# Kernel optimization log

Hardware: AMD Instinct MI355X
Metric: run time of the kernel (lower is better)

Reference implementation:

```python
import jax, jax.numpy as jnp
import numpy as np

NUM_GENES = 5000
EMBED = 64
HID = 64
FEATS = 64
SLOPE = 0.01  # nn.LeakyReLU default
BN_EPS = 1e-5


def setup_inputs() -> dict:
    key = jax.random.key(0)
    ks = jax.random.split(key, 20)
    N, E = 40000, 1280000
    def w(k, shape):
        return jax.random.normal(k, shape, dtype=jnp.float32) * 0.05
    inp = {
        "x": jax.random.normal(ks[0], (N, FEATS), dtype=jnp.float32),
        "edge_index": jax.random.randint(ks[1], (2, E), 0, N, dtype=jnp.int64),
        # pre_mp Linear(num_feats, hidden)
        "W_pre": w(ks[2], (FEATS, HID)), "b_pre": w(ks[3], (HID,)),
        # conv 0 MLP: Linear->LeakyReLU->Linear
        "c0_W1": w(ks[4], (HID, HID)), "c0_b1": w(ks[5], (HID,)),
        "c0_W2": w(ks[6], (HID, HID)), "c0_b2": w(ks[7], (HID,)),
        # bn 0 (only bns[0] is used since last conv has no bn)
        "bn0_g": jnp.ones((HID,), jnp.float32), "bn0_b": jnp.zeros((HID,), jnp.float32),
        # conv 1 MLP
        "c1_W1": w(ks[8], (HID, HID)), "c1_b1": w(ks[9], (HID,)),
        "c1_W2": w(ks[10], (HID, HID)), "c1_b2": w(ks[11], (HID,)),
        # post_mp: Linear(hid,hid)->LeakyReLU->Linear(hid,embed)
        "Wp1": w(ks[12], (HID, HID)), "bp1": w(ks[13], (HID,)),
        "Wp2": w(ks[14], (HID, EMBED)), "bp2": w(ks[15], (EMBED,)),
    }
    return inp


def _gin_conv(x, src, dst, W1, b1, W2, b2):
    # GINConv, eps=0: MLP(x + sum_{j in N(i)} x_j)
    agg = jax.ops.segment_sum(x[src], dst, num_segments=x.shape[0])
    h = x + agg
    h = jax.nn.leaky_relu(h @ W1 + b1, SLOPE) @ W2 + b2
    return h


def _batchnorm(h, g, b):
    mu = h.mean(axis=0)
    var = ((h - mu) ** 2).mean(axis=0)  # biased, training-mode BN
    return (h - mu) * jax.lax.rsqrt(var + BN_EPS) * g + b


def reference(x, edge_index, W_pre, b_pre, c0_W1, c0_b1, c0_W2, c0_b2,
              bn0_g, bn0_b, c1_W1, c1_b1, c1_W2, c1_b2, Wp1, bp1, Wp2, bp2):
    src, dst = edge_index[0], edge_index[1]
    h = x @ W_pre + b_pre                                  # [N, HID]
    h = _gin_conv(h, src, dst, c0_W1, c0_b1, c0_W2, c0_b2)
    h = _batchnorm(h, bn0_g, bn0_b)
    h = _gin_conv(h, src, dst, c1_W1, c1_b1, c1_W2, c1_b2)  # last conv, no bn
    h = jax.nn.leaky_relu(h @ Wp1 + bp1, SLOPE) @ Wp2 + bp2  # [N, EMBED]
    # flatten + split into per-graph chunks of num_genes*embed, then stack
    return h.reshape(-1, NUM_GENES * EMBED)                 # [B, 5000*64]
```

## Files before the change

kernel.cpp:

```cpp
#include <hip/hip_runtime.h>
#include <hip/hip_fp16.h>

constexpr float SLOPE  = 0.01f;
constexpr float BN_EPS = 1e-5f;
constexpr int   CAP    = 96;
constexpr int   CLAMP  = 80;
constexpr int   NXCD   = 8;
constexpr int   EPB    = 2048;

__device__ inline void acc8(const uint4& v, float* a) {
    float2 f;
    f = __half22float2(*(const __half2*)&v.x); a[0] += f.x; a[1] += f.y;
    f = __half22float2(*(const __half2*)&v.y); a[2] += f.x; a[3] += f.y;
    f = __half22float2(*(const __half2*)&v.z); a[4] += f.x; a[5] += f.y;
    f = __half22float2(*(const __half2*)&v.w); a[6] += f.x; a[7] += f.y;
}

__global__ void k_fill_linear(const int* __restrict__ src, const int* __restrict__ dst,
                              int* __restrict__ cnt, unsigned short* __restrict__ ssrc, int E,
                              const float* __restrict__ x, const float* __restrict__ W,
                              const float* __restrict__ bias, __half* __restrict__ H0,
                              int total, int fillBlocks, int N, int Npart) {
    int bid = blockIdx.x;
    if (bid < fillBlocks) {
        int p     = bid & (NXCD - 1);
        int chunk = bid >> 3;
        int lo = p * Npart;
        int hi = min(N, lo + Npart);
        int base = chunk * EPB;
#pragma unroll
        for (int i = 0; i < EPB / 256; ++i) {
            int e = base + i * 256 + (int)threadIdx.x;
            if (e < E) {
                int d = dst[e];
                if (d >= lo && d < hi) {
                    int pos = atomicAdd(&cnt[d], 1);
                    if (pos < CAP) ssrc[(size_t)d * CAP + pos] = (unsigned short)src[e];
                }
            }
        }
    } else {
        int gid = (bid - fillBlocks) * 256 + threadIdx.x;
        if (gid < total) {
            int n = gid >> 6, f = gid & 63;
            const float* row = x + (size_t)n * 64;
            float acc = bias[f];
#pragma unroll
            for (int k = 0; k < 64; ++k) acc = fmaf(row[k], W[k * 64 + f], acc);
            H0[gid] = __float2half(acc);
        }
    }
}

#define GLD(j) \
    uint4 vA##j, vB##j; \
    { int jA = sidx[g][((j) << 4) + sub]; \
      int jB = sidx[g][((j) << 4) + 8 + sub]; \
      vA##j = in16[(size_t)jA * 8 + q]; \
      vB##j = in16[(size_t)jB * 8 + q]; }
#define GACC(j) do { acc8(vA##j, a); acc8(vB##j, a); } while (0)

template <bool BN_IN, bool DO_POST, typename TO>
__global__ void k_conv8(const __half* __restrict__ in, const int* __restrict__ cnt,
                        const unsigned short* __restrict__ ssrc,
                        const float* __restrict__ stats, const float* __restrict__ gm,
                        const float* __restrict__ bt, float invN,
                        const float* __restrict__ W1, const float* __restrict__ b1,
                        const float* __restrict__ W2, const float* __restrict__ b2,
                        const float* __restrict__ Wp1, const float* __restrict__ bp1,
                        const float* __restrict__ Wp2, const float* __restrict__ bp2,
                        TO* __restrict__ out, int N, int nblk) {
    __shared__ unsigned short sidx[4][CAP];
    __shared__ float row[4][64];
    __shared__ float t[4][64];
    __shared__ float csc[64], csh[64];

    int bid = blockIdx.x;
    int q8 = nblk / NXCD, r8 = nblk % NXCD;
    int xcd = bid % NXCD, sl = bid / NXCD;
    int wg = (xcd < r8 ? xcd * (q8 + 1) : r8 * (q8 + 1) + (xcd - r8) * q8) + sl;
    int n0 = wg * 4;

    int tid = threadIdx.x;
    int lane = tid & 63, g = tid >> 6;
    int n = n0 + g;
    bool act = n < N;
    int sub = lane >> 3;
    int q   = lane & 7;

    if constexpr (BN_IN) {
        if (tid < 64) {
            float mu  = stats[tid] * invN;
            float var = stats[64 + tid] * invN - mu * mu;
            float sc  = rsqrtf(var + BN_EPS) * gm[tid];
            csc[tid] = sc;
            csh[tid] = bt[tid] - mu * sc;
        }
        __syncthreads();
    }

    if (act) {
        const uint4* in16 = (const uint4*)in;
        int c  = min(cnt[n], CLAMP);
        c = __builtin_amdgcn_readfirstlane(c);
        int cp = (c + 15) & ~15;
        int iters = cp >> 4;

        const unsigned short* bkt = ssrc + (size_t)n * CAP;
        unsigned short self = (unsigned short)n;
        if (lane < cp) sidx[g][lane] = (lane < c) ? bkt[lane] : self;
        int p2 = lane + 64;
        if (p2 < cp) sidx[g][p2] = (p2 < c) ? bkt[p2] : self;

        uint4 vs = make_uint4(0, 0, 0, 0);
        if (sub == 0) vs = in16[(size_t)n * 8 + q];

        float a[8] = {0.f, 0.f, 0.f, 0.f, 0.f, 0.f, 0.f, 0.f};
        switch (iters) {
        case 1: { GLD(0) GACC(0); } break;
        case 2: { GLD(0) GLD(1) GACC(0); GACC(1); } break;
        case 3: { GLD(0) GLD(1) GLD(2) GACC(0); GACC(1); GACC(2); } break;
        case 4: { GLD(0) GLD(1) GLD(2) GACC(0); GLD(3) GACC(1); GACC(2); GACC(3); } break;
        case 5: { GLD(0) GLD(1) GLD(2) GACC(0); GLD(3) GACC(1); GLD(4) GACC(2);
                  GACC(3); GACC(4); } break;
        default: break;
        }
#pragma unroll
        for (int k = 0; k < 8; ++k) {
            a[k] += __shfl_xor(a[k], 8);
            a[k] += __shfl_xor(a[k], 16);
            a[k] += __shfl_xor(a[k], 32);
        }
        if (sub == 0) {
            float ws = 1.0f - (float)(cp - c);
            float2 f;
            f = __half22float2(*(const __half2*)&vs.x); a[0] = fmaf(ws, f.x, a[0]); a[1] = fmaf(ws, f.y, a[1]);
            f = __half22float2(*(const __half2*)&vs.y); a[2] = fmaf(ws, f.x, a[2]); a[3] = fmaf(ws, f.y, a[3]);
            f = __half22float2(*(const __half2*)&vs.z); a[4] = fmaf(ws, f.x, a[4]); a[5] = fmaf(ws, f.y, a[5]);
            f = __half22float2(*(const __half2*)&vs.w); a[6] = fmaf(ws, f.x, a[6]); a[7] = fmaf(ws, f.y, a[7]);
            int f0 = q * 8;
            if constexpr (BN_IN) {
                float dp1 = (float)(c + 1);
#pragma unroll
                for (int k = 0; k < 8; ++k) a[k] = fmaf(csc[f0 + k], a[k], dp1 * csh[f0 + k]);
            }
            *(float4*)&row[g][f0]     = make_float4(a[0], a[1], a[2], a[3]);
            *(float4*)&row[g][f0 + 4] = make_float4(a[4], a[5], a[6], a[7]);
        }

        float a1 = b1[lane];
#pragma unroll
        for (int k0 = 0; k0 < 16; ++k0) {
            float4 r = *(const float4*)&row[g][k0 * 4];
            a1 = fmaf(r.x, W1[(k0 * 4 + 0) * 64 + lane], a1);
            a1 = fmaf(r.y, W1[(k0 * 4 + 1) * 64 + lane], a1);
            a1 = fmaf(r.z, W1[(k0 * 4 + 2) * 64 + lane], a1);
            a1 = fmaf(r.w, W1[(k0 * 4 + 3) * 64 + lane], a1);
        }
        t[g][lane] = a1 > 0.f ? a1 : SLOPE * a1;

        float a2 = b2[lane];
#pragma unroll
        for (int k0 = 0; k0 < 16; ++k0) {
            float4 r = *(const float4*)&t[g][k0 * 4];
            a2 = fmaf(r.x, W2[(k0 * 4 + 0) * 64 + lane], a2);
            a2 = fmaf(r.y, W2[(k0 * 4 + 1) * 64 + lane], a2);
            a2 = fmaf(r.z, W2[(k0 * 4 + 2) * 64 + lane], a2);
            a2 = fmaf(r.w, W2[(k0 * 4 + 3) * 64 + lane], a2);
        }
        if constexpr (!DO_POST) {
            out[(size_t)n * 64 + lane] = (TO)a2;
        } else {
            row[g][lane] = a2;
            float a3 = bp1[lane];
#pragma unroll
            for (int k0 = 0; k0 < 16; ++k0) {
                float4 r = *(const float4*)&row[g][k0 * 4];
                a3 = fmaf(r.x, Wp1[(k0 * 4 + 0) * 64 + lane], a3);
                a3 = fmaf(r.y, Wp1[(k0 * 4 + 1) * 64 + lane], a3);
                a3 = fmaf(r.z, Wp1[(k0 * 4 + 2) * 64 + lane], a3);
                a3 = fmaf(r.w, Wp1[(k0 * 4 + 3) * 64 + lane], a3);
            }
            t[g][lane] = a3 > 0.f ? a3 : SLOPE * a3;

            float a4 = bp2[lane];
#pragma unroll
            for (int k0 = 0; k0 < 16; ++k0) {
                float4 r = *(const float4*)&t[g][k0 * 4];
                a4 = fmaf(r.x, Wp2[(k0 * 4 + 0) * 64 + lane], a4);
                a4 = fmaf(r.y, Wp2[(k0 * 4 + 1) * 64 + lane], a4);
                a4 = fmaf(r.z, Wp2[(k0 * 4 + 2) * 64 + lane], a4);
                a4 = fmaf(r.w, Wp2[(k0 * 4 + 3) * 64 + lane], a4);
            }
            out[(size_t)n * 64 + lane] = (TO)a4;
        }
    }
}

__global__ void k_bn_stats_h(const __half* __restrict__ h, float* __restrict__ stats, int N) {
    int f = threadIdx.x & 63, g = threadIdx.x >> 6;
    float s = 0.f, ss = 0.f;
    for (int r = blockIdx.x * 4 + g; r < N; r += gridDim.x * 4) {
        float v = __half2float(h[(size_t)r * 64 + f]);
        s += v;
        ss += v * v;
    }
    __shared__ float sh[2][256];
    sh[0][threadIdx.x] = s;
    sh[1][threadIdx.x] = ss;
    __syncthreads();
    if (g == 0) {
        s  = sh[0][f] + sh[0][f + 64] + sh[0][f + 128] + sh[0][f + 192];
        ss = sh[1][f] + sh[1][f + 64] + sh[1][f + 128] + sh[1][f + 192];
        atomicAdd(&stats[f], s);
        atomicAdd(&stats[64 + f], ss);
    }
}

__global__ void k_linear_f(const float* __restrict__ in, const float* __restrict__ W,
                           const float* __restrict__ bias, float* __restrict__ out, int total) {
    int gid = blockIdx.x * blockDim.x + threadIdx.x;
    if (gid >= total) return;
    int n = gid >> 6, f = gid & 63;
    const float* row = in + (size_t)n * 64;
    float acc = bias[f];
#pragma unroll
    for (int k = 0; k < 64; ++k) acc = fmaf(row[k], W[k * 64 + f], acc);
    out[gid] = acc;
}

__global__ void k_scatter(const float* __restrict__ h, const int* __restrict__ src,
                          const int* __restrict__ dst, float* __restrict__ agg, int E) {
    long long gid = (long long)blockIdx.x * blockDim.x + threadIdx.x;
    if (gid >= (long long)E * 64) return;
    int e = (int)(gid >> 6);
    int f = (int)(gid & 63);
    atomicAdd(&agg[(size_t)dst[e] * 64 + f], h[(size_t)src[e] * 64 + f]);
}

__global__ void k_mlp2(const float* __restrict__ in, const float* __restrict__ agg,
                       const float* __restrict__ W1, const float* __restrict__ b1,
                       const float* __restrict__ W2, const float* __restrict__ b2,
                       float* __restrict__ out, int N) {
    __shared__ float row[4][64];
    __shared__ float t[4][64];
    int f = threadIdx.x & 63, g = threadIdx.x >> 6;
    int n = blockIdx.x * 4 + g;
    bool act = n < N;
    if (act) {
        float v = in[(size_t)n * 64 + f];
        if (agg) v += agg[(size_t)n * 64 + f];
        row[g][f] = v;
    }
    __syncthreads();
    if (act) {
        float acc = b1[f];
#pragma unroll
        for (int k = 0; k < 64; ++k) acc = fmaf(row[g][k], W1[k * 64 + f], acc);
        t[g][f] = acc > 0.f ? acc : SLOPE * acc;
    }
    __syncthreads();
    if (act) {
        float acc = b2[f];
#pragma unroll
        for (int k = 0; k < 64; ++k) acc = fmaf(t[g][k], W2[k * 64 + f], acc);
        out[(size_t)n * 64 + f] = acc;
    }
}

__global__ void k_bn_stats_f(const float* __restrict__ h, float* __restrict__ stats, int N) {
    int f = threadIdx.x & 63, g = threadIdx.x >> 6;
    float s = 0.f, ss = 0.f;
    for (int r = blockIdx.x * 4 + g; r < N; r += gridDim.x * 4) {
        float v = h[(size_t)r * 64 + f];
        s += v;
        ss += v * v;
    }
    __shared__ float sh[2][256];
    sh[0][threadIdx.x] = s;
    sh[1][threadIdx.x] = ss;
    __syncthreads();
    if (g == 0) {
        s  = sh[0][f] + sh[0][f + 64] + sh[0][f + 128] + sh[0][f + 192];
        ss = sh[1][f] + sh[1][f + 64] + sh[1][f + 128] + sh[1][f + 192];
        atomicAdd(&stats[f], s);
        atomicAdd(&stats[64 + f], ss);
    }
}

__global__ void k_bn_apply(float* __restrict__ h, const float* __restrict__ stats,
                           const float* __restrict__ gm, const float* __restrict__ bt,
                           int total, float invN) {
    int gid = blockIdx.x * blockDim.x + threadIdx.x;
    if (gid >= total) return;
    int f = gid & 63;
    float mu  = stats[f] * invN;
    float var = stats[64 + f] * invN - mu * mu;
    float sc  = rsqrtf(var + BN_EPS) * gm[f];
    h[gid] = (h[gid] - mu) * sc + bt[f];
}

extern "C" void kernel_launch(void* const* d_in, const int* in_sizes, int n_in,
                              void* d_out, int out_size, void* d_ws, size_t ws_size,
                              hipStream_t stream) {
    const float* x      = (const float*)d_in[0];
    const int*   ei     = (const int*)d_in[1];
    const float* W_pre  = (const float*)d_in[2];
    const float* b_pre  = (const float*)d_in[3];
    const float* c0_W1  = (const float*)d_in[4];
    const float* c0_b1  = (const float*)d_in[5];
    const float* c0_W2  = (const float*)d_in[6];
    const float* c0_b2  = (const float*)d_in[7];
    const float* bn0_g  = (const float*)d_in[8];
    const float* bn0_b  = (const float*)d_in[9];
    const float* c1_W1  = (const float*)d_in[10];
    const float* c1_b1  = (const float*)d_in[11];
    const float* c1_W2  = (const float*)d_in[12];
    const float* c1_b2  = (const float*)d_in[13];
    const float* Wp1    = (const float*)d_in[14];
    const float* bp1    = (const float*)d_in[15];
    const float* Wp2    = (const float*)d_in[16];
    const float* bp2    = (const float*)d_in[17];

    const int N = in_sizes[0] / 64;
    const int E = in_sizes[1] / 2;
    const int total = N * 64;
    const float invN = 1.0f / (float)N;

    const int* src = ei;
    const int* dst = ei + E;

    dim3 blk(256);
    dim3 grid_n((N + 3) / 4);
    int nblk = (N + 3) / 4;
    int Npart = (N + NXCD - 1) / NXCD;
    int fillBlocks = ((E + EPB - 1) / EPB) * NXCD;
    int linBlocks  = (total + 255) / 256;

    char* w = (char*)d_ws;
    __half* H1 = (__half*)w;                     w += (size_t)total * 2;
    w = (char*)(((size_t)w + 255) & ~(size_t)255);
    unsigned short* ssrc = (unsigned short*)w;   w += (size_t)N * CAP * 2 + 128;
    w = (char*)(((size_t)w + 255) & ~(size_t)255);
    int* cnt = (int*)w;                          w += (size_t)N * 4;
    float* stats = (float*)w;                    w += 128 * 4;
    size_t needed = (size_t)(w - (char*)d_ws);

    if (ws_size >= needed) {
        __half* H0 = (__half*)d_out;
        hipMemsetAsync(cnt, 0, (size_t)N * 4, stream);
        k_fill_linear<<<dim3(fillBlocks + linBlocks), blk, 0, stream>>>(
            src, dst, cnt, ssrc, E, x, W_pre, b_pre, H0, total, fillBlocks, N, Npart);
        k_conv8<false, false, __half><<<grid_n, blk, 0, stream>>>(
            H0, cnt, ssrc, nullptr, nullptr, nullptr, 0.f,
            c0_W1, c0_b1, c0_W2, c0_b2, nullptr, nullptr, nullptr, nullptr, H1, N, nblk);
        hipMemsetAsync(stats, 0, 128 * 4, stream);
        k_bn_stats_h<<<dim3(256), blk, 0, stream>>>(H1, stats, N);
        k_conv8<true, true, float><<<grid_n, blk, 0, stream>>>(
            H1, cnt, ssrc, stats, bn0_g, bn0_b, invN,
            c1_W1, c1_b1, c1_W2, c1_b2, Wp1, bp1, Wp2, bp2, (float*)d_out, N, nblk);
    } else {
        float* A   = (float*)d_out;
        float* B   = (float*)d_ws;
        float* st2 = B + (size_t)total;
        dim3 grid_nf((total + 255) / 256);
        dim3 grid_ef((unsigned)(((long long)E * 64 + 255) / 256));
        k_linear_f<<<grid_nf, blk, 0, stream>>>(x, W_pre, b_pre, A, total);
        hipMemsetAsync(B, 0, (size_t)total * 4, stream);
        k_scatter<<<grid_ef, blk, 0, stream>>>(A, src, dst, B, E);
        k_mlp2<<<grid_n, blk, 0, stream>>>(A, B, c0_W1, c0_b1, c0_W2, c0_b2, A, N);
        hipMemsetAsync(st2, 0, 128 * 4, stream);
        k_bn_stats_f<<<dim3(1024), blk, 0, stream>>>(A, st2, N);
        k_bn_apply<<<grid_nf, blk, 0, stream>>>(A, st2, bn0_g, bn0_b, total, invN);
        hipMemsetAsync(B, 0, (size_t)total * 4, stream);
        k_scatter<<<grid_ef, blk, 0, stream>>>(A, src, dst, B, E);
        k_mlp2<<<grid_n, blk, 0, stream>>>(A, B, c1_W1, c1_b1, c1_W2, c1_b2, A, N);
        k_mlp2<<<grid_n, blk, 0, stream>>>(A, nullptr, Wp1, bp1, Wp2, bp2, A, N);
    }
}
```

Baseline: 250.0 us.

## Replicate half-precision node features per XCD to localize gather traffic

Producers of H0 and H1 now write eight copies of each feature matrix, one per XCD. Each conv block gathers neighbor rows from the copy indexed by its XCD (blockIdx % 8), so random neighbor reads should stay within that XCD's L2 instead of pulling lines cached on other dies. The cost is eight times the write traffic for the linear and first-conv outputs, plus a larger workspace requirement. A single-copy fallback path is kept for when the workspace is too small.

```diff
diff --git a/kernel.cpp b/kernel.cpp
--- a/kernel.cpp
+++ b/kernel.cpp
@@ -20,6 +20,7 @@
                               int* __restrict__ cnt, unsigned short* __restrict__ ssrc, int E,
                               const float* __restrict__ x, const float* __restrict__ W,
                               const float* __restrict__ bias, __half* __restrict__ H0,
+                              size_t h0Stride, int h0Reps,
                               int total, int fillBlocks, int N, int Npart) {
     int bid = blockIdx.x;
     if (bid < fillBlocks) {
@@ -47,7 +48,8 @@
             float acc = bias[f];
 #pragma unroll
             for (int k = 0; k < 64; ++k) acc = fmaf(row[k], W[k * 64 + f], acc);
-            H0[gid] = __float2half(acc);
+            __half hv = __float2half(acc);
+            for (int r = 0; r < h0Reps; ++r) H0[(size_t)r * h0Stride + gid] = hv;
         }
     }
 }
@@ -61,7 +63,8 @@
 #define GACC(j) do { acc8(vA##j, a); acc8(vB##j, a); } while (0)
 
 template <bool BN_IN, bool DO_POST, typename TO>
-__global__ void k_conv8(const __half* __restrict__ in, const int* __restrict__ cnt,
+__global__ void k_conv9(const __half* __restrict__ in, size_t inRepStride,
+                        const int* __restrict__ cnt,
                         const unsigned short* __restrict__ ssrc,
                         const float* __restrict__ stats, const float* __restrict__ gm,
                         const float* __restrict__ bt, float invN,
@@ -69,15 +72,17 @@
                         const float* __restrict__ W2, const float* __restrict__ b2,
                         const float* __restrict__ Wp1, const float* __restrict__ bp1,
                         const float* __restrict__ Wp2, const float* __restrict__ bp2,
-                        TO* __restrict__ out, int N, int nblk) {
+                        TO* __restrict__ out, size_t outRepStride, int outReps,
+                        int N, int nblk) {
     __shared__ unsigned short sidx[4][CAP];
     __shared__ float row[4][64];
     __shared__ float t[4][64];
     __shared__ float csc[64], csh[64];
 
     int bid = blockIdx.x;
+    int xcd = bid % NXCD;
     int q8 = nblk / NXCD, r8 = nblk % NXCD;
-    int xcd = bid % NXCD, sl = bid / NXCD;
+    int sl = bid / NXCD;
     int wg = (xcd < r8 ? xcd * (q8 + 1) : r8 * (q8 + 1) + (xcd - r8) * q8) + sl;
     int n0 = wg * 4;
 
@@ -100,7 +105,7 @@
     }
 
     if (act) {
-        const uint4* in16 = (const uint4*)in;
+        const uint4* in16 = (const uint4*)(in + (size_t)xcd * inRepStride);
         int c  = min(cnt[n], CLAMP);
         c = __builtin_amdgcn_readfirstlane(c);
         int cp = (c + 15) & ~15;
@@ -169,7 +174,9 @@
             a2 = fmaf(r.w, W2[(k0 * 4 + 3) * 64 + lane], a2);
         }
         if constexpr (!DO_POST) {
-            out[(size_t)n * 64 + lane] = (TO)a2;
+            TO v = (TO)a2;
+            for (int r = 0; r < outReps; ++r)
+                out[(size_t)r * outRepStride + (size_t)n * 64 + lane] = v;
         } else {
             row[g][lane] = a2;
             float a3 = bp1[lane];
@@ -192,16 +199,20 @@
                 a4 = fmaf(r.z, Wp2[(k0 * 4 + 2) * 64 + lane], a4);
                 a4 = fmaf(r.w, Wp2[(k0 * 4 + 3) * 64 + lane], a4);
             }
-            out[(size_t)n * 64 + lane] = (TO)a4;
-        }
-    }
-}
-
-__global__ void k_bn_stats_h(const __half* __restrict__ h, float* __restrict__ stats, int N) {
+            TO v = (TO)a4;
+            for (int r = 0; r < outReps; ++r)
+                out[(size_t)r * outRepStride + (size_t)n * 64 + lane] = v;
+        }
+    }
+}
+
+__global__ void k_bn_stats_h(const __half* __restrict__ h, size_t repStride,
+                             float* __restrict__ stats, int N) {
+    const __half* hh = h + (size_t)(blockIdx.x % NXCD) * repStride;
     int f = threadIdx.x & 63, g = threadIdx.x >> 6;
     float s = 0.f, ss = 0.f;
     for (int r = blockIdx.x * 4 + g; r < N; r += gridDim.x * 4) {
-        float v = __half2float(h[(size_t)r * 64 + f]);
+        float v = __half2float(hh[(size_t)r * 64 + f]);
         s += v;
         ss += v * v;
     }
@@ -337,28 +348,58 @@
     int fillBlocks = ((E + EPB - 1) / EPB) * NXCD;
     int linBlocks  = (total + 255) / 256;
 
-    char* w = (char*)d_ws;
-    __half* H1 = (__half*)w;                     w += (size_t)total * 2;
-    w = (char*)(((size_t)w + 255) & ~(size_t)255);
-    unsigned short* ssrc = (unsigned short*)w;   w += (size_t)N * CAP * 2 + 128;
-    w = (char*)(((size_t)w + 255) & ~(size_t)255);
-    int* cnt = (int*)w;                          w += (size_t)N * 4;
-    float* stats = (float*)w;                    w += 128 * 4;
-    size_t needed = (size_t)(w - (char*)d_ws);
-
-    if (ws_size >= needed) {
+    size_t repBytes   = (size_t)NXCD * total * 2;
+    size_t bucketsB   = (size_t)N * CAP * 2 + 256;
+    size_t cntB       = (size_t)N * 4;
+    size_t needRep    = 2 * repBytes + bucketsB + cntB + 1024;
+    size_t needSingle = (size_t)total * 2 + bucketsB + cntB + 1024;
+
+    if (ws_size >= needRep) {
+        char* w = (char*)d_ws;
+        __half* H0 = (__half*)w;                     w += repBytes;
+        __half* H1 = (__half*)w;                     w += repBytes;
+        unsigned short* ssrc = (unsigned short*)w;   w += bucketsB;
+        w = (char*)(((size_t)w + 255) & ~(size_t)255);
+        int* cnt = (int*)w;                          w += cntB;
+        float* stats = (float*)w;
+
+        hipMemsetAsync(cnt, 0, cntB, stream);
+        k_fill_linear<<<dim3(fillBlocks + linBlocks), blk, 0, stream>>>(
+            src, dst, cnt, ssrc, E, x, W_pre, b_pre, H0, (size_t)total, NXCD,
+            total, fillBlocks, N, Npart);
+        k_conv9<false, false, __half><<<grid_n, blk, 0, stream>>>(
+            H0, (size_t)total, cnt, ssrc, nullptr, nullptr, nullptr, 0.f,
+            c0_W1, c0_b1, c0_W2, c0_b2, nullptr, nullptr, nullptr, nullptr,
+            H1, (size_t)total, NXCD, N, nblk);
+        hipMemsetAsync(stats, 0, 128 * 4, stream);
+        k_bn_stats_h<<<dim3(256), blk, 0, stream>>>(H1, (size_t)total, stats, N);
+        k_conv9<true, true, float><<<grid_n, blk, 0, stream>>>(
+            H1, (size_t)total, cnt, ssrc, stats, bn0_g, bn0_b, invN,
+            c1_W1, c1_b1, c1_W2, c1_b2, Wp1, bp1, Wp2, bp2,
+            (float*)d_out, 0, 1, N, nblk);
+    } else if (ws_size >= needSingle) {
+        char* w = (char*)d_ws;
+        __half* H1 = (__half*)w;                     w += (size_t)total * 2;
+        unsigned short* ssrc = (unsigned short*)w;   w += bucketsB;
+        w = (char*)(((size_t)w + 255) & ~(size_t)255);
+        int* cnt = (int*)w;                          w += cntB;
+        float* stats = (float*)w;
+
         __half* H0 = (__half*)d_out;
-        hipMemsetAsync(cnt, 0, (size_t)N * 4, stream);
+        hipMemsetAsync(cnt, 0, cntB, stream);
         k_fill_linear<<<dim3(fillBlocks + linBlocks), blk, 0, stream>>>(
-            src, dst, cnt, ssrc, E, x, W_pre, b_pre, H0, total, fillBlocks, N, Npart);
-        k_conv8<false, false, __half><<<grid_n, blk, 0, stream>>>(
-            H0, cnt, ssrc, nullptr, nullptr, nullptr, 0.f,
-            c0_W1, c0_b1, c0_W2, c0_b2, nullptr, nullptr, nullptr, nullptr, H1, N, nblk);
+            src, dst, cnt, ssrc, E, x, W_pre, b_pre, H0, 0, 1,
+            total, fillBlocks, N, Npart);
+        k_conv9<false, false, __half><<<grid_n, blk, 0, stream>>>(
+            H0, 0, cnt, ssrc, nullptr, nullptr, nullptr, 0.f,
+            c0_W1, c0_b1, c0_W2, c0_b2, nullptr, nullptr, nullptr, nullptr,
+            H1, 0, 1, N, nblk);
         hipMemsetAsync(stats, 0, 128 * 4, stream);
-        k_bn_stats_h<<<dim3(256), blk, 0, stream>>>(H1, stats, N);
-        k_conv8<true, true, float><<<grid_n, blk, 0, stream>>>(
-            H1, cnt, ssrc, stats, bn0_g, bn0_b, invN,
-            c1_W1, c1_b1, c1_W2, c1_b2, Wp1, bp1, Wp2, bp2, (float*)d_out, N, nblk);
+        k_bn_stats_h<<<dim3(256), blk, 0, stream>>>(H1, 0, stats, N);
+        k_conv9<true, true, float><<<grid_n, blk, 0, stream>>>(
+            H1, 0, cnt, ssrc, stats, bn0_g, bn0_b, invN,
+            c1_W1, c1_b1, c1_W2, c1_b2, Wp1, bp1, Wp2, bp2,
+            (float*)d_out, 0, 1, N, nblk);
     } else {
         float* A   = (float*)d_out;
         float* B   = (float*)d_ws;
```

After: 267.1 us. 1.07x slower.
